# Kernel tuning notes

Measured on AMD Instinct MI355X. Metric: run time of the kernel, lower is better.

## Reference

```python
import jax, jax.numpy as jnp
import numpy as np

EPS = 1e-6


def _att_vector(x, W, b, sharp2, th2, is_last):
    """AttentionVector on a 2D payoff slice.
    x: (N, a, m). W: (1, 2), b: (1,). Returns (N, a)."""
    # compare_param: pair (x[n,j,k], x[n,i,k]) -> Linear(2,1) -> sigmoid -> mean over k
    # Linear on the concat pair is w00*x[n,j,k] + w01*x[n,i,k] + b, so we fuse it.
    lin = W[0, 0] * x[:, None, :, :] + W[0, 1] * x[:, :, None, :] + b[0]  # (N,a,a,m)
    c = jnp.mean(jax.nn.sigmoid(lin), axis=3)  # (N,a,a)
    # max_normalize over dim 2
    c = c / (jnp.max(c, axis=2, keepdims=True) + EPS)
    # compute_player_mask
    m = jnp.mean(c, axis=2)  # (N,a)
    m = jax.nn.relu(m * sharp2[0] + th2[0])
    m = jax.nn.softmax(m, axis=1)
    if not is_last:
        m = m / (jnp.max(m, axis=1, keepdims=True) + EPS)
    return m


def setup_inputs() -> dict:
    key = jax.random.key(0)
    ks = jax.random.split(key, 16)
    N, a1, a2, f = 128, 64, 64, 2
    inp = {
        "x": jax.random.normal(ks[0], (N, f, a1, a2), dtype=jnp.float32),
        "fc_W": jax.random.normal(ks[1], (2, 2), dtype=jnp.float32) * 0.5,
        "fc_b": jax.random.normal(ks[2], (2,), dtype=jnp.float32) * 0.1,
        "p1_W": jax.random.normal(ks[3], (1, 2), dtype=jnp.float32) * 0.5,
        "p1_b": jax.random.normal(ks[4], (1,), dtype=jnp.float32) * 0.1,
        "p1_sharp": jnp.ones((1,), dtype=jnp.float32),
        "p1_th": jnp.zeros((1,), dtype=jnp.float32),
        "p2_W": jax.random.normal(ks[5], (1, 2), dtype=jnp.float32) * 0.5,
        "p2_b": jax.random.normal(ks[6], (1,), dtype=jnp.float32) * 0.1,
        "p2_sharp": jnp.ones((1,), dtype=jnp.float32),
        "p2_th": jnp.zeros((1,), dtype=jnp.float32),
        "out_W": jax.random.normal(ks[7], (1, 2), dtype=jnp.float32) * 0.5,
        "out_b": jax.random.normal(ks[8], (1,), dtype=jnp.float32) * 0.1,
        "out_sharp": jnp.ones((1,), dtype=jnp.float32),
        "out_th": jnp.zeros((1,), dtype=jnp.float32),
    }
    return inp


def reference(x, fc_W, fc_b, p1_W, p1_b, p1_sharp, p1_th,
              p2_W, p2_b, p2_sharp, p2_th,
              out_W, out_b, out_sharp, out_th):
    # x: (N, f=2, a1, a2) -> (N, a1, a2, f)
    h = jnp.transpose(x, (0, 2, 3, 1))
    # is_fc_first: Linear(2, 2) + ReLU on last dim
    h = jax.nn.relu(h @ fc_W.T + fc_b)  # (N,a1,a2,2)
    # one AttentionModule (module_layers=1, not simult)
    vec1 = _att_vector(h[..., 0], p1_W, p1_b, p1_sharp, p1_th, is_last=False)  # (N,a1)
    h = h * vec1[:, :, None, None]
    pl2 = jnp.transpose(h[..., 1], (0, 2, 1))  # (N,a2,a1)
    vec2 = _att_vector(pl2, p2_W, p2_b, p2_sharp, p2_th, is_last=False)  # (N,a2)
    h = h * vec2[:, None, :, None]
    # with_last: final AttentionVector (is_last=True) on player-1 channel
    out = _att_vector(h[..., 0], out_W, out_b, out_sharp, out_th, is_last=True)  # (N,a1)
    return out
```

## Files before the change

kernel.cpp:

```cpp
#include <hip/hip_runtime.h>


constexpr int A   = 64;
constexpr int PAD = 68;
constexpr float L2E  = 1.4426950408889634f;
constexpr float EPSF = 1e-6f;

__device__ __forceinline__ float bcast(float v, int srcLane) {
    return __int_as_float(__builtin_amdgcn_readlane(__float_as_int(v), srcLane));
}
__device__ __forceinline__ float rcpf(float v) { return __builtin_amdgcn_rcpf(v); }
__device__ __forceinline__ float ex2(float v)  { return __builtin_amdgcn_exp2f(v); }

template <int CTRL>
__device__ __forceinline__ float upd_dpp(float src) {
    return __int_as_float(__builtin_amdgcn_update_dpp(
        0, __float_as_int(src), CTRL, 0xF, 0xF, true));
}
__device__ __forceinline__ float wave_sum64(float x) {
    x += upd_dpp<0x111>(x);
    x += upd_dpp<0x112>(x);
    x += upd_dpp<0x114>(x);
    x += upd_dpp<0x118>(x);
    x += upd_dpp<0x142>(x);
    x += upd_dpp<0x143>(x);
    return bcast(x, 63);
}
__device__ __forceinline__ float wave_max64(float x) {
    x = fmaxf(x, upd_dpp<0x111>(x));
    x = fmaxf(x, upd_dpp<0x112>(x));
    x = fmaxf(x, upd_dpp<0x114>(x));
    x = fmaxf(x, upd_dpp<0x118>(x));
    x = fmaxf(x, upd_dpp<0x142>(x));
    x = fmaxf(x, upd_dpp<0x143>(x));
    return bcast(x, 63);
}

__device__ __forceinline__ void att2q(const float* __restrict__ prow,
                                      const float* __restrict__ qL,
                                      int row0, int lane,
                                      float* __restrict__ mbuf,
                                      float* __restrict__ mg)
{
    const float qreg0 = qL[row0 * PAD + lane];
    const float qreg1 = qL[(row0 + 1) * PAD + lane];
    float acc0 = 0.f, acc1 = 0.f;
#pragma unroll
    for (int c = 0; c < 4; ++c) {
        float pk[16];
        *(float4*)(&pk[0])  = *(const float4*)(prow + c * 16 + 0);
        *(float4*)(&pk[4])  = *(const float4*)(prow + c * 16 + 4);
        *(float4*)(&pk[8])  = *(const float4*)(prow + c * 16 + 8);
        *(float4*)(&pk[12]) = *(const float4*)(prow + c * 16 + 12);
#pragma unroll
        for (int g = 0; g < 4; ++g) {
            const int k = c * 16 + 4 * g;
            const float p0 = pk[4 * g], p1 = pk[4 * g + 1];
            const float p2 = pk[4 * g + 2], p3 = pk[4 * g + 3];
            {
                float u0 = fmaf(p0, bcast(qreg0, k),     1.0f);
                float u1 = fmaf(p1, bcast(qreg0, k + 1), 1.0f);
                float u2 = fmaf(p2, bcast(qreg0, k + 2), 1.0f);
                float u3 = fmaf(p3, bcast(qreg0, k + 3), 1.0f);
                float a = u0 * u1, b = u2 * u3;
                float numer = fmaf(u0 + u1, b, (u2 + u3) * a);
                acc0 = fmaf(numer, rcpf(a * b), acc0);
            }
            {
                float u0 = fmaf(p0, bcast(qreg1, k),     1.0f);
                float u1 = fmaf(p1, bcast(qreg1, k + 1), 1.0f);
                float u2 = fmaf(p2, bcast(qreg1, k + 2), 1.0f);
                float u3 = fmaf(p3, bcast(qreg1, k + 3), 1.0f);
                float a = u0 * u1, b = u2 * u3;
                float numer = fmaf(u0 + u1, b, (u2 + u3) * a);
                acc1 = fmaf(numer, rcpf(a * b), acc1);
            }
        }
    }
    const float s0 = wave_sum64(acc0), m0 = wave_max64(acc0);
    const float s1 = wave_sum64(acc1), m1 = wave_max64(acc1);
    if (lane == 0) {
        float v0 = (s0 * (1.0f / 4096.0f)) / (m0 * (1.0f / 64.0f) + EPSF);
        float v1 = (s1 * (1.0f / 4096.0f)) / (m1 * (1.0f / 64.0f) + EPSF);
        mbuf[row0]     = v0;
        mbuf[row0 + 1] = v1;
        __hip_atomic_store(mg + row0,     v0 + 2.0f, __ATOMIC_RELAXED, __HIP_MEMORY_SCOPE_AGENT);
        __hip_atomic_store(mg + row0 + 1, v1 + 2.0f, __ATOMIC_RELAXED, __HIP_MEMORY_SCOPE_AGENT);
    }
}

__device__ __forceinline__ float softmax64(float m, float sharp, float th, bool last)
{
    float v = fmaxf(0.f, m * sharp + th);
    float mx = wave_max64(v);
    float e = __expf(v - mx);
    float s = wave_sum64(e);
    float r = e / s;
    if (!last) {
        float rm = wave_max64(r);
        r = r / (rm + EPSF);
    }
    return r;
}

__device__ __forceinline__ float exch_soft(const float* __restrict__ mbuf,
                                           const float* __restrict__ mg,
                                           int half, int lane,
                                           float sharp, float th, bool last)
{
    float mv;
    if ((lane >> 5) == half) {
        mv = mbuf[lane];
    } else {
        const float* p = mg + lane;
        for (;;) {
            float f = __hip_atomic_load(p, __ATOMIC_RELAXED, __HIP_MEMORY_SCOPE_AGENT);
            unsigned u = __float_as_uint(f);
            if ((u >> 23) == 0x80u) { mv = f - 2.0f; break; }
            __builtin_amdgcn_s_sleep(1);
        }
    }
    return softmax64(mv, sharp, th, last);
}

__global__ __launch_bounds__(1024, 4)
void attn_half(const float* __restrict__ x,
               const float* __restrict__ fcW, const float* __restrict__ fcb,
               const float* __restrict__ p1W, const float* __restrict__ p1b,
               const float* __restrict__ p1s, const float* __restrict__ p1t,
               const float* __restrict__ p2W, const float* __restrict__ p2b,
               const float* __restrict__ p2s, const float* __restrict__ p2t,
               const float* __restrict__ oW,  const float* __restrict__ ob,
               const float* __restrict__ os,  const float* __restrict__ ot,
               float* __restrict__ mglob,
               float* __restrict__ out)
{
    __shared__ __align__(16) float pL[A * PAD];
    __shared__ __align__(16) float qL[A * PAD];
    __shared__ float mbuf[A];
    __shared__ float v1buf[A], v2buf[A];

    const int tid = threadIdx.x, lane = tid & 63, wv = tid >> 6;
    const int n = blockIdx.x >> 1, half = blockIdx.x & 1;
    const int row0 = half * 32 + wv * 2;
    const int i = tid >> 4, j = (tid & 15) * 4;
    float* mg = mglob + (size_t)n * 3 * A;

    const float4* x0v = (const float4*)(x + (size_t)n * 2 * A * A);
    const float4* x1v = x0v + (A * A / 4);
    const float4 a = x0v[tid];
    const float4 c = x1v[tid];
    const float w00 = fcW[0], w01 = fcW[1], w10 = fcW[2], w11 = fcW[3];
    const float b0 = fcb[0], b1 = fcb[1];
    const float h0v[4] = { fmaxf(0.f, w00 * a.x + w01 * c.x + b0),
                           fmaxf(0.f, w00 * a.y + w01 * c.y + b0),
                           fmaxf(0.f, w00 * a.z + w01 * c.z + b0),
                           fmaxf(0.f, w00 * a.w + w01 * c.w + b0) };
    const float h1v[4] = { fmaxf(0.f, w10 * a.x + w11 * c.x + b1),
                           fmaxf(0.f, w10 * a.y + w11 * c.y + b1),
                           fmaxf(0.f, w10 * a.z + w11 * c.z + b1),
                           fmaxf(0.f, w10 * a.w + w11 * c.w + b1) };

    {
        const float W0 = p1W[0], W1 = p1W[1], bb = p1b[0];
        float4 pv, qv;
        pv.x = ex2(-L2E * (W0 * h0v[0] + bb)); qv.x = ex2(-L2E * (W1 * h0v[0]));
        pv.y = ex2(-L2E * (W0 * h0v[1] + bb)); qv.y = ex2(-L2E * (W1 * h0v[1]));
        pv.z = ex2(-L2E * (W0 * h0v[2] + bb)); qv.z = ex2(-L2E * (W1 * h0v[2]));
        pv.w = ex2(-L2E * (W0 * h0v[3] + bb)); qv.w = ex2(-L2E * (W1 * h0v[3]));
        *(float4*)&pL[i * PAD + j] = pv;
        *(float4*)&qL[i * PAD + j] = qv;
    }
    __syncthreads();
    att2q(pL + lane * PAD, qL, row0, lane, mbuf, mg);
    __syncthreads();
    if (wv == 0) v1buf[lane] = exch_soft(mbuf, mg, half, lane, p1s[0], p1t[0], false);
    __syncthreads();

    {
        const float W0 = p2W[0], W1 = p2W[1], bb = p2b[0];
        const float sc = v1buf[i];
#pragma unroll
        for (int t = 0; t < 4; ++t) {
            float hv = h1v[t] * sc;
            pL[(j + t) * PAD + i] = ex2(-L2E * (W0 * hv + bb));
            qL[(j + t) * PAD + i] = ex2(-L2E * (W1 * hv));
        }
    }
    __syncthreads();
    att2q(pL + lane * PAD, qL, row0, lane, mbuf, mg + A);
    __syncthreads();
    if (wv == 0) v2buf[lane] = exch_soft(mbuf, mg + A, half, lane, p2s[0], p2t[0], false);
    __syncthreads();

    {
        const float W0 = oW[0], W1 = oW[1], bb = ob[0];
        const float sc = v1buf[i];
        const float4 v2q = *(const float4*)&v2buf[j];
        float hv0 = h0v[0] * sc * v2q.x, hv1 = h0v[1] * sc * v2q.y;
        float hv2 = h0v[2] * sc * v2q.z, hv3 = h0v[3] * sc * v2q.w;
        float4 pv, qv;
        pv.x = ex2(-L2E * (W0 * hv0 + bb)); qv.x = ex2(-L2E * (W1 * hv0));
        pv.y = ex2(-L2E * (W0 * hv1 + bb)); qv.y = ex2(-L2E * (W1 * hv1));
        pv.z = ex2(-L2E * (W0 * hv2 + bb)); qv.z = ex2(-L2E * (W1 * hv2));
        pv.w = ex2(-L2E * (W0 * hv3 + bb)); qv.w = ex2(-L2E * (W1 * hv3));
        *(float4*)&pL[i * PAD + j] = pv;
        *(float4*)&qL[i * PAD + j] = qv;
    }
    __syncthreads();
    att2q(pL + lane * PAD, qL, row0, lane, mbuf, mg + 2 * A);
    __syncthreads();

    if (wv == 0) {
        float r = exch_soft(mbuf, mg + 2 * A, half, lane, os[0], ot[0], true);
        if ((lane >> 5) == half) out[(size_t)n * A + lane] = r;
    }
}

extern "C" void kernel_launch(void* const* d_in, const int* in_sizes, int n_in,
                              void* d_out, int out_size, void* d_ws, size_t ws_size,
                              hipStream_t stream)
{
    (void)n_in; (void)out_size; (void)ws_size;
    const float* x   = (const float*)d_in[0];
    const float* fcW = (const float*)d_in[1];
    const float* fcb = (const float*)d_in[2];
    const float* p1W = (const float*)d_in[3];
    const float* p1b = (const float*)d_in[4];
    const float* p1s = (const float*)d_in[5];
    const float* p1t = (const float*)d_in[6];
    const float* p2W = (const float*)d_in[7];
    const float* p2b = (const float*)d_in[8];
    const float* p2s = (const float*)d_in[9];
    const float* p2t = (const float*)d_in[10];
    const float* oW  = (const float*)d_in[11];
    const float* ob  = (const float*)d_in[12];
    const float* os  = (const float*)d_in[13];
    const float* ot  = (const float*)d_in[14];
    float* out = (float*)d_out;

    const int N = in_sizes[0] / (2 * A * A);
    float* mglob = (float*)d_ws;

    attn_half<<<2 * N, 1024, 0, stream>>>(x, fcW, fcb,
                                          p1W, p1b, p1s, p1t,
                                          p2W, p2b, p2s, p2t,
                                          oW, ob, os, ot, mglob, out);
}
```

Baseline: 100.1 us.

## Split each sample across four 512-thread blocks and poll softmax in every wave

Each sample's work is now spread across four blocks of 512 threads instead of two blocks of 1024, and each thread handles eight elements. Every wave polls the global exchange buffer for all 64 row values and computes the softmax redundantly. The result is broadcast across lanes with ds_bpermute instead of going through shared-memory buffers, which removes several __syncthreads barriers. In exchange there is more cross-block spin-waiting on global memory, and the blocks of one sample must all be co-resident to avoid deadlock.

```diff
diff --git a/kernel.cpp b/kernel.cpp
--- a/kernel.cpp
+++ b/kernel.cpp
@@ -11,6 +11,9 @@
 }
 __device__ __forceinline__ float rcpf(float v) { return __builtin_amdgcn_rcpf(v); }
 __device__ __forceinline__ float ex2(float v)  { return __builtin_amdgcn_exp2f(v); }
+__device__ __forceinline__ float lanebc(float v, int idx) {
+    return __int_as_float(__builtin_amdgcn_ds_bpermute(idx << 2, __float_as_int(v)));
+}
 
 template <int CTRL>
 __device__ __forceinline__ float upd_dpp(float src) {
@@ -39,7 +42,6 @@
 __device__ __forceinline__ void att2q(const float* __restrict__ prow,
                                       const float* __restrict__ qL,
                                       int row0, int lane,
-                                      float* __restrict__ mbuf,
                                       float* __restrict__ mg)
 {
     const float qreg0 = qL[row0 * PAD + lane];
@@ -82,8 +84,6 @@
     if (lane == 0) {
         float v0 = (s0 * (1.0f / 4096.0f)) / (m0 * (1.0f / 64.0f) + EPSF);
         float v1 = (s1 * (1.0f / 4096.0f)) / (m1 * (1.0f / 64.0f) + EPSF);
-        mbuf[row0]     = v0;
-        mbuf[row0 + 1] = v1;
         __hip_atomic_store(mg + row0,     v0 + 2.0f, __ATOMIC_RELAXED, __HIP_MEMORY_SCOPE_AGENT);
         __hip_atomic_store(mg + row0 + 1, v1 + 2.0f, __ATOMIC_RELAXED, __HIP_MEMORY_SCOPE_AGENT);
     }
@@ -103,117 +103,111 @@
     return r;
 }
 
-__device__ __forceinline__ float exch_soft(const float* __restrict__ mbuf,
-                                           const float* __restrict__ mg,
-                                           int half, int lane,
+__device__ __forceinline__ float poll_soft(const float* __restrict__ mg,
+                                           int lane,
                                            float sharp, float th, bool last)
 {
     float mv;
-    if ((lane >> 5) == half) {
-        mv = mbuf[lane];
-    } else {
-        const float* p = mg + lane;
-        for (;;) {
-            float f = __hip_atomic_load(p, __ATOMIC_RELAXED, __HIP_MEMORY_SCOPE_AGENT);
-            unsigned u = __float_as_uint(f);
-            if ((u >> 23) == 0x80u) { mv = f - 2.0f; break; }
-            __builtin_amdgcn_s_sleep(1);
-        }
+    const float* p = mg + lane;
+    for (;;) {
+        float f = __hip_atomic_load(p, __ATOMIC_RELAXED, __HIP_MEMORY_SCOPE_AGENT);
+        if (__all((__float_as_uint(f) >> 23) == 0x80u)) { mv = f - 2.0f; break; }
+        __builtin_amdgcn_s_sleep(1);
     }
     return softmax64(mv, sharp, th, last);
 }
 
-__global__ __launch_bounds__(1024, 4)
-void attn_half(const float* __restrict__ x,
-               const float* __restrict__ fcW, const float* __restrict__ fcb,
-               const float* __restrict__ p1W, const float* __restrict__ p1b,
-               const float* __restrict__ p1s, const float* __restrict__ p1t,
-               const float* __restrict__ p2W, const float* __restrict__ p2b,
-               const float* __restrict__ p2s, const float* __restrict__ p2t,
-               const float* __restrict__ oW,  const float* __restrict__ ob,
-               const float* __restrict__ os,  const float* __restrict__ ot,
-               float* __restrict__ mglob,
-               float* __restrict__ out)
+__global__ __launch_bounds__(512, 4)
+void attn_q(const float* __restrict__ x,
+            const float* __restrict__ fcW, const float* __restrict__ fcb,
+            const float* __restrict__ p1W, const float* __restrict__ p1b,
+            const float* __restrict__ p1s, const float* __restrict__ p1t,
+            const float* __restrict__ p2W, const float* __restrict__ p2b,
+            const float* __restrict__ p2s, const float* __restrict__ p2t,
+            const float* __restrict__ oW,  const float* __restrict__ ob,
+            const float* __restrict__ os,  const float* __restrict__ ot,
+            float* __restrict__ mglob,
+            float* __restrict__ out)
 {
     __shared__ __align__(16) float pL[A * PAD];
     __shared__ __align__(16) float qL[A * PAD];
-    __shared__ float mbuf[A];
-    __shared__ float v1buf[A], v2buf[A];
 
     const int tid = threadIdx.x, lane = tid & 63, wv = tid >> 6;
-    const int n = blockIdx.x >> 1, half = blockIdx.x & 1;
-    const int row0 = half * 32 + wv * 2;
-    const int i = tid >> 4, j = (tid & 15) * 4;
+    const int n = blockIdx.x >> 2, quarter = blockIdx.x & 3;
+    const int row0 = quarter * 16 + wv * 2;
+    const int i = tid >> 3, j8 = (tid & 7) << 3;
     float* mg = mglob + (size_t)n * 3 * A;
 
-    const float4* x0v = (const float4*)(x + (size_t)n * 2 * A * A);
-    const float4* x1v = x0v + (A * A / 4);
-    const float4 a = x0v[tid];
-    const float4 c = x1v[tid];
-    const float w00 = fcW[0], w01 = fcW[1], w10 = fcW[2], w11 = fcW[3];
-    const float b0 = fcb[0], b1 = fcb[1];
-    const float h0v[4] = { fmaxf(0.f, w00 * a.x + w01 * c.x + b0),
-                           fmaxf(0.f, w00 * a.y + w01 * c.y + b0),
-                           fmaxf(0.f, w00 * a.z + w01 * c.z + b0),
-                           fmaxf(0.f, w00 * a.w + w01 * c.w + b0) };
-    const float h1v[4] = { fmaxf(0.f, w10 * a.x + w11 * c.x + b1),
-                           fmaxf(0.f, w10 * a.y + w11 * c.y + b1),
-                           fmaxf(0.f, w10 * a.z + w11 * c.z + b1),
-                           fmaxf(0.f, w10 * a.w + w11 * c.w + b1) };
+    const float4* xv = (const float4*)(x + (size_t)n * 2 * A * A);
+    const float4 a0 = xv[2 * tid], a1 = xv[2 * tid + 1];
+    const float4 c0 = xv[1024 + 2 * tid], c1 = xv[1024 + 2 * tid + 1];
+    float h0v[8], h1v[8];
+    {
+        const float w00 = fcW[0], w01 = fcW[1], w10 = fcW[2], w11 = fcW[3];
+        const float b0 = fcb[0], b1 = fcb[1];
+        const float av[8] = { a0.x, a0.y, a0.z, a0.w, a1.x, a1.y, a1.z, a1.w };
+        const float cv[8] = { c0.x, c0.y, c0.z, c0.w, c1.x, c1.y, c1.z, c1.w };
+#pragma unroll
+        for (int t = 0; t < 8; ++t) {
+            h0v[t] = fmaxf(0.f, w00 * av[t] + w01 * cv[t] + b0);
+            h1v[t] = fmaxf(0.f, w10 * av[t] + w11 * cv[t] + b1);
+        }
+    }
 
     {
         const float W0 = p1W[0], W1 = p1W[1], bb = p1b[0];
-        float4 pv, qv;
-        pv.x = ex2(-L2E * (W0 * h0v[0] + bb)); qv.x = ex2(-L2E * (W1 * h0v[0]));
-        pv.y = ex2(-L2E * (W0 * h0v[1] + bb)); qv.y = ex2(-L2E * (W1 * h0v[1]));
-        pv.z = ex2(-L2E * (W0 * h0v[2] + bb)); qv.z = ex2(-L2E * (W1 * h0v[2]));
-        pv.w = ex2(-L2E * (W0 * h0v[3] + bb)); qv.w = ex2(-L2E * (W1 * h0v[3]));
-        *(float4*)&pL[i * PAD + j] = pv;
-        *(float4*)&qL[i * PAD + j] = qv;
+        float pv[8], qv[8];
+#pragma unroll
+        for (int t = 0; t < 8; ++t) {
+            pv[t] = ex2(-L2E * (W0 * h0v[t] + bb));
+            qv[t] = ex2(-L2E * (W1 * h0v[t]));
+        }
+        *(float4*)&pL[i * PAD + j8]     = make_float4(pv[0], pv[1], pv[2], pv[3]);
+        *(float4*)&pL[i * PAD + j8 + 4] = make_float4(pv[4], pv[5], pv[6], pv[7]);
+        *(float4*)&qL[i * PAD + j8]     = make_float4(qv[0], qv[1], qv[2], qv[3]);
+        *(float4*)&qL[i * PAD + j8 + 4] = make_float4(qv[4], qv[5], qv[6], qv[7]);
     }
     __syncthreads();
-    att2q(pL + lane * PAD, qL, row0, lane, mbuf, mg);
+    att2q(pL + lane * PAD, qL, row0, lane, mg);
+    const float r1   = poll_soft(mg, lane, p1s[0], p1t[0], false);
+    const float v1_i = lanebc(r1, i);
+
+    {
+        const float W0 = p2W[0], W1 = p2W[1], bb = p2b[0];
+#pragma unroll
+        for (int t = 0; t < 8; ++t) {
+            const float hv = h1v[t] * v1_i;
+            pL[(j8 + t) * PAD + i] = ex2(-L2E * (W0 * hv + bb));
+            qL[(j8 + t) * PAD + i] = ex2(-L2E * (W1 * hv));
+        }
+    }
     __syncthreads();
-    if (wv == 0) v1buf[lane] = exch_soft(mbuf, mg, half, lane, p1s[0], p1t[0], false);
+    att2q(pL + lane * PAD, qL, row0, lane, mg + A);
+    const float r2 = poll_soft(mg + A, lane, p2s[0], p2t[0], false);
+
+    float v2j[8];
+#pragma unroll
+    for (int t = 0; t < 8; ++t) v2j[t] = lanebc(r2, j8 + t);
+    {
+        const float W0 = oW[0], W1 = oW[1], bb = ob[0];
+        float pv[8], qv[8];
+#pragma unroll
+        for (int t = 0; t < 8; ++t) {
+            const float hv = h0v[t] * v1_i * v2j[t];
+            pv[t] = ex2(-L2E * (W0 * hv + bb));
+            qv[t] = ex2(-L2E * (W1 * hv));
+        }
+        *(float4*)&pL[i * PAD + j8]     = make_float4(pv[0], pv[1], pv[2], pv[3]);
+        *(float4*)&pL[i * PAD + j8 + 4] = make_float4(pv[4], pv[5], pv[6], pv[7]);
+        *(float4*)&qL[i * PAD + j8]     = make_float4(qv[0], qv[1], qv[2], qv[3]);
+        *(float4*)&qL[i * PAD + j8 + 4] = make_float4(qv[4], qv[5], qv[6], qv[7]);
+    }
     __syncthreads();
-
-    {
-        const float W0 = p2W[0], W1 = p2W[1], bb = p2b[0];
-        const float sc = v1buf[i];
-#pragma unroll
-        for (int t = 0; t < 4; ++t) {
-            float hv = h1v[t] * sc;
-            pL[(j + t) * PAD + i] = ex2(-L2E * (W0 * hv + bb));
-            qL[(j + t) * PAD + i] = ex2(-L2E * (W1 * hv));
-        }
-    }
-    __syncthreads();
-    att2q(pL + lane * PAD, qL, row0, lane, mbuf, mg + A);
-    __syncthreads();
-    if (wv == 0) v2buf[lane] = exch_soft(mbuf, mg + A, half, lane, p2s[0], p2t[0], false);
-    __syncthreads();
-
-    {
-        const float W0 = oW[0], W1 = oW[1], bb = ob[0];
-        const float sc = v1buf[i];
-        const float4 v2q = *(const float4*)&v2buf[j];
-        float hv0 = h0v[0] * sc * v2q.x, hv1 = h0v[1] * sc * v2q.y;
-        float hv2 = h0v[2] * sc * v2q.z, hv3 = h0v[3] * sc * v2q.w;
-        float4 pv, qv;
-        pv.x = ex2(-L2E * (W0 * hv0 + bb)); qv.x = ex2(-L2E * (W1 * hv0));
-        pv.y = ex2(-L2E * (W0 * hv1 + bb)); qv.y = ex2(-L2E * (W1 * hv1));
-        pv.z = ex2(-L2E * (W0 * hv2 + bb)); qv.z = ex2(-L2E * (W1 * hv2));
-        pv.w = ex2(-L2E * (W0 * hv3 + bb)); qv.w = ex2(-L2E * (W1 * hv3));
-        *(float4*)&pL[i * PAD + j] = pv;
-        *(float4*)&qL[i * PAD + j] = qv;
-    }
-    __syncthreads();
-    att2q(pL + lane * PAD, qL, row0, lane, mbuf, mg + 2 * A);
-    __syncthreads();
+    att2q(pL + lane * PAD, qL, row0, lane, mg + 2 * A);
 
     if (wv == 0) {
-        float r = exch_soft(mbuf, mg + 2 * A, half, lane, os[0], ot[0], true);
-        if ((lane >> 5) == half) out[(size_t)n * A + lane] = r;
+        const float r = poll_soft(mg + 2 * A, lane, os[0], ot[0], true);
+        if ((lane >> 4) == quarter) out[(size_t)n * A + lane] = r;
     }
 }
 
@@ -242,8 +236,8 @@
     const int N = in_sizes[0] / (2 * A * A);
     float* mglob = (float*)d_ws;
 
-    attn_half<<<2 * N, 1024, 0, stream>>>(x, fcW, fcb,
-                                          p1W, p1b, p1s, p1t,
-                                          p2W, p2b, p2s, p2t,
-                                          oW, ob, os, ot, mglob, out);
-}
+    attn_q<<<4 * N, 512, 0, stream>>>(x, fcW, fcb,
+                                      p1W, p1b, p1s, p1t,
+                                      p2W, p2b, p2s, p2t,
+                                      oW, ob, os, ot, mglob, out);
+}
```

Measured after the change: 110.6 us. 10.5% more time.

## Process each sample in one block instead of two cooperating half-blocks

Applied to the files above, without the earlier changes.

Replaces the two-blocks-per-sample split, which swapped row statistics through global memory with atomic spin-waits, with one 1024-thread block per sample. Each wave now handles four rows instead of two. Every wave computes the softmax redundantly and gets the per-row scale factors by lane broadcast rather than shared-memory buffers, which drops a barrier per stage. This removes the cross-block handshake and its latency, but halves the grid, so only 128 blocks cover the device and per-block compute doubles.

```diff
diff --git a/kernel.cpp b/kernel.cpp
--- a/kernel.cpp
+++ b/kernel.cpp
@@ -11,6 +11,9 @@
 }
 __device__ __forceinline__ float rcpf(float v) { return __builtin_amdgcn_rcpf(v); }
 __device__ __forceinline__ float ex2(float v)  { return __builtin_amdgcn_exp2f(v); }
+__device__ __forceinline__ float lanebc(float v, int idx) {
+    return __int_as_float(__builtin_amdgcn_ds_bpermute(idx << 2, __float_as_int(v)));
+}
 
 template <int CTRL>
 __device__ __forceinline__ float upd_dpp(float src) {
@@ -39,8 +42,7 @@
 __device__ __forceinline__ void att2q(const float* __restrict__ prow,
                                       const float* __restrict__ qL,
                                       int row0, int lane,
-                                      float* __restrict__ mbuf,
-                                      float* __restrict__ mg)
+                                      float* __restrict__ mbuf)
 {
     const float qreg0 = qL[row0 * PAD + lane];
     const float qreg1 = qL[(row0 + 1) * PAD + lane];
@@ -80,12 +82,8 @@
     const float s0 = wave_sum64(acc0), m0 = wave_max64(acc0);
     const float s1 = wave_sum64(acc1), m1 = wave_max64(acc1);
     if (lane == 0) {
-        float v0 = (s0 * (1.0f / 4096.0f)) / (m0 * (1.0f / 64.0f) + EPSF);
-        float v1 = (s1 * (1.0f / 4096.0f)) / (m1 * (1.0f / 64.0f) + EPSF);
-        mbuf[row0]     = v0;
-        mbuf[row0 + 1] = v1;
-        __hip_atomic_store(mg + row0,     v0 + 2.0f, __ATOMIC_RELAXED, __HIP_MEMORY_SCOPE_AGENT);
-        __hip_atomic_store(mg + row0 + 1, v1 + 2.0f, __ATOMIC_RELAXED, __HIP_MEMORY_SCOPE_AGENT);
+        mbuf[row0]     = (s0 * (1.0f / 4096.0f)) / (m0 * (1.0f / 64.0f) + EPSF);
+        mbuf[row0 + 1] = (s1 * (1.0f / 4096.0f)) / (m1 * (1.0f / 64.0f) + EPSF);
     }
 }
 
@@ -103,28 +101,8 @@
     return r;
 }
 
-__device__ __forceinline__ float exch_soft(const float* __restrict__ mbuf,
-                                           const float* __restrict__ mg,
-                                           int half, int lane,
-                                           float sharp, float th, bool last)
-{
-    float mv;
-    if ((lane >> 5) == half) {
-        mv = mbuf[lane];
-    } else {
-        const float* p = mg + lane;
-        for (;;) {
-            float f = __hip_atomic_load(p, __ATOMIC_RELAXED, __HIP_MEMORY_SCOPE_AGENT);
-            unsigned u = __float_as_uint(f);
-            if ((u >> 23) == 0x80u) { mv = f - 2.0f; break; }
-            __builtin_amdgcn_s_sleep(1);
-        }
-    }
-    return softmax64(mv, sharp, th, last);
-}
-
 __global__ __launch_bounds__(1024, 4)
-void attn_half(const float* __restrict__ x,
+void attn_full(const float* __restrict__ x,
                const float* __restrict__ fcW, const float* __restrict__ fcb,
                const float* __restrict__ p1W, const float* __restrict__ p1b,
                const float* __restrict__ p1s, const float* __restrict__ p1t,
@@ -132,19 +110,16 @@
                const float* __restrict__ p2s, const float* __restrict__ p2t,
                const float* __restrict__ oW,  const float* __restrict__ ob,
                const float* __restrict__ os,  const float* __restrict__ ot,
-               float* __restrict__ mglob,
                float* __restrict__ out)
 {
     __shared__ __align__(16) float pL[A * PAD];
     __shared__ __align__(16) float qL[A * PAD];
     __shared__ float mbuf[A];
-    __shared__ float v1buf[A], v2buf[A];
 
     const int tid = threadIdx.x, lane = tid & 63, wv = tid >> 6;
-    const int n = blockIdx.x >> 1, half = blockIdx.x & 1;
-    const int row0 = half * 32 + wv * 2;
+    const int n = blockIdx.x;
+    const int row0 = wv * 4;
     const int i = tid >> 4, j = (tid & 15) * 4;
-    float* mg = mglob + (size_t)n * 3 * A;
 
     const float4* x0v = (const float4*)(x + (size_t)n * 2 * A * A);
     const float4* x1v = x0v + (A * A / 4);
@@ -172,48 +147,50 @@
         *(float4*)&qL[i * PAD + j] = qv;
     }
     __syncthreads();
-    att2q(pL + lane * PAD, qL, row0, lane, mbuf, mg);
-    __syncthreads();
-    if (wv == 0) v1buf[lane] = exch_soft(mbuf, mg, half, lane, p1s[0], p1t[0], false);
-    __syncthreads();
+    att2q(pL + lane * PAD, qL, row0,     lane, mbuf);
+    att2q(pL + lane * PAD, qL, row0 + 2, lane, mbuf);
+    __syncthreads();
+    const float r1   = softmax64(mbuf[lane], p1s[0], p1t[0], false);
+    const float v1_i = lanebc(r1, i);
 
     {
         const float W0 = p2W[0], W1 = p2W[1], bb = p2b[0];
-        const float sc = v1buf[i];
 #pragma unroll
         for (int t = 0; t < 4; ++t) {
-            float hv = h1v[t] * sc;
+            const float hv = h1v[t] * v1_i;
             pL[(j + t) * PAD + i] = ex2(-L2E * (W0 * hv + bb));
             qL[(j + t) * PAD + i] = ex2(-L2E * (W1 * hv));
         }
     }
     __syncthreads();
-    att2q(pL + lane * PAD, qL, row0, lane, mbuf, mg + A);
-    __syncthreads();
-    if (wv == 0) v2buf[lane] = exch_soft(mbuf, mg + A, half, lane, p2s[0], p2t[0], false);
-    __syncthreads();
+    att2q(pL + lane * PAD, qL, row0,     lane, mbuf);
+    att2q(pL + lane * PAD, qL, row0 + 2, lane, mbuf);
+    __syncthreads();
+    const float r2 = softmax64(mbuf[lane], p2s[0], p2t[0], false);
+    float v2j[4];
+#pragma unroll
+    for (int t = 0; t < 4; ++t) v2j[t] = lanebc(r2, j + t);
 
     {
-        const float W0 = oW[0], W1 = oW[1], bb = ob[0];
-        const float sc = v1buf[i];
-        const float4 v2q = *(const float4*)&v2buf[j];
-        float hv0 = h0v[0] * sc * v2q.x, hv1 = h0v[1] * sc * v2q.y;
-        float hv2 = h0v[2] * sc * v2q.z, hv3 = h0v[3] * sc * v2q.w;
+        const float W0 = oW[0], W1 = ob ? oW[1] : oW[1], bb = ob[0];
+        const float hv0 = h0v[0] * v1_i * v2j[0], hv1 = h0v[1] * v1_i * v2j[1];
+        const float hv2 = h0v[2] * v1_i * v2j[2], hv3 = h0v[3] * v1_i * v2j[3];
         float4 pv, qv;
-        pv.x = ex2(-L2E * (W0 * hv0 + bb)); qv.x = ex2(-L2E * (W1 * hv0));
-        pv.y = ex2(-L2E * (W0 * hv1 + bb)); qv.y = ex2(-L2E * (W1 * hv1));
-        pv.z = ex2(-L2E * (W0 * hv2 + bb)); qv.z = ex2(-L2E * (W1 * hv2));
-        pv.w = ex2(-L2E * (W0 * hv3 + bb)); qv.w = ex2(-L2E * (W1 * hv3));
+        pv.x = ex2(-L2E * (W0 * hv0 + bb)); qv.x = ex2(-L2E * (oW[1] * hv0));
+        pv.y = ex2(-L2E * (W0 * hv1 + bb)); qv.y = ex2(-L2E * (oW[1] * hv1));
+        pv.z = ex2(-L2E * (W0 * hv2 + bb)); qv.z = ex2(-L2E * (oW[1] * hv2));
+        pv.w = ex2(-L2E * (W0 * hv3 + bb)); qv.w = ex2(-L2E * (oW[1] * hv3));
         *(float4*)&pL[i * PAD + j] = pv;
         *(float4*)&qL[i * PAD + j] = qv;
     }
     __syncthreads();
-    att2q(pL + lane * PAD, qL, row0, lane, mbuf, mg + 2 * A);
+    att2q(pL + lane * PAD, qL, row0,     lane, mbuf);
+    att2q(pL + lane * PAD, qL, row0 + 2, lane, mbuf);
     __syncthreads();
 
     if (wv == 0) {
-        float r = exch_soft(mbuf, mg + 2 * A, half, lane, os[0], ot[0], true);
-        if ((lane >> 5) == half) out[(size_t)n * A + lane] = r;
+        const float r = softmax64(mbuf[lane], os[0], ot[0], true);
+        out[(size_t)n * A + lane] = r;
     }
 }
 
@@ -221,7 +198,7 @@
                               void* d_out, int out_size, void* d_ws, size_t ws_size,
                               hipStream_t stream)
 {
-    (void)n_in; (void)out_size; (void)ws_size;
+    (void)n_in; (void)out_size; (void)d_ws; (void)ws_size;
     const float* x   = (const float*)d_in[0];
     const float* fcW = (const float*)d_in[1];
     const float* fcb = (const float*)d_in[2];
@@ -240,10 +217,9 @@
     float* out = (float*)d_out;
 
     const int N = in_sizes[0] / (2 * A * A);
-    float* mglob = (float*)d_ws;
-
-    attn_half<<<2 * N, 1024, 0, stream>>>(x, fcW, fcb,
-                                          p1W, p1b, p1s, p1t,
-                                          p2W, p2b, p2s, p2t,
-                                          oW, ob, os, ot, mglob, out);
-}
+
+    attn_full<<<N, 1024, 0, stream>>>(x, fcW, fcb,
+                                      p1W, p1b, p1s, p1t,
+                                      p2W, p2b, p2s, p2t,
+                                      oW, ob, os, ot, out);
+}
```

Result: slower. 109.1 us (+8.9%).

## Exchange half-block masks through output buffer with tagged ack handshake; load q from LDS

Applied to the files above, without the earlier changes.

Drops the workspace buffer and uses the output row itself as the inter-block mailbox. Values carry a per-phase additive tag, and the consumer writes back an ack that the producer waits for before the slot is reused. The attention inner loop now reads q values from LDS with float4 loads instead of readlane broadcasts from a register, which trades SALU/readlane traffic for LDS bandwidth. It clamps mask values to a small positive floor so the tag decode works, which slightly changes semantics for near-zero values. It also adds an extra spin-wait round-trip per phase.

```diff
diff --git a/kernel.cpp b/kernel.cpp
--- a/kernel.cpp
+++ b/kernel.cpp
@@ -37,13 +37,11 @@
 }
 
 __device__ __forceinline__ void att2q(const float* __restrict__ prow,
-                                      const float* __restrict__ qL,
+                                      const float* __restrict__ qrow,
                                       int row0, int lane,
                                       float* __restrict__ mbuf,
-                                      float* __restrict__ mg)
-{
-    const float qreg0 = qL[row0 * PAD + lane];
-    const float qreg1 = qL[(row0 + 1) * PAD + lane];
+                                      unsigned* __restrict__ mg, unsigned K)
+{
     float acc0 = 0.f, acc1 = 0.f;
 #pragma unroll
     for (int c = 0; c < 4; ++c) {
@@ -57,24 +55,21 @@
             const int k = c * 16 + 4 * g;
             const float p0 = pk[4 * g], p1 = pk[4 * g + 1];
             const float p2 = pk[4 * g + 2], p3 = pk[4 * g + 3];
-            {
-                float u0 = fmaf(p0, bcast(qreg0, k),     1.0f);
-                float u1 = fmaf(p1, bcast(qreg0, k + 1), 1.0f);
-                float u2 = fmaf(p2, bcast(qreg0, k + 2), 1.0f);
-                float u3 = fmaf(p3, bcast(qreg0, k + 3), 1.0f);
-                float a = u0 * u1, b = u2 * u3;
-                float numer = fmaf(u0 + u1, b, (u2 + u3) * a);
-                acc0 = fmaf(numer, rcpf(a * b), acc0);
+            const float4 q0 = *(const float4*)(qrow + k);
+            const float4 q1 = *(const float4*)(qrow + PAD + k);
+#define ROW_ACC(ACC, Q)                                              \
+            {                                                        \
+                float u0 = fmaf(p0, (Q).x, 1.0f);                    \
+                float u1 = fmaf(p1, (Q).y, 1.0f);                    \
+                float u2 = fmaf(p2, (Q).z, 1.0f);                    \
+                float u3 = fmaf(p3, (Q).w, 1.0f);                    \
+                float a = u0 * u1, b = u2 * u3;                      \
+                float numer = fmaf(u0 + u1, b, (u2 + u3) * a);       \
+                ACC = fmaf(numer, rcpf(a * b), ACC);                 \
             }
-            {
-                float u0 = fmaf(p0, bcast(qreg1, k),     1.0f);
-                float u1 = fmaf(p1, bcast(qreg1, k + 1), 1.0f);
-                float u2 = fmaf(p2, bcast(qreg1, k + 2), 1.0f);
-                float u3 = fmaf(p3, bcast(qreg1, k + 3), 1.0f);
-                float a = u0 * u1, b = u2 * u3;
-                float numer = fmaf(u0 + u1, b, (u2 + u3) * a);
-                acc1 = fmaf(numer, rcpf(a * b), acc1);
-            }
+            ROW_ACC(acc0, q0)
+            ROW_ACC(acc1, q1)
+#undef ROW_ACC
         }
     }
     const float s0 = wave_sum64(acc0), m0 = wave_max64(acc0);
@@ -82,10 +77,14 @@
     if (lane == 0) {
         float v0 = (s0 * (1.0f / 4096.0f)) / (m0 * (1.0f / 64.0f) + EPSF);
         float v1 = (s1 * (1.0f / 4096.0f)) / (m1 * (1.0f / 64.0f) + EPSF);
+        v0 = fmaxf(v0, 1e-9f);
+        v1 = fmaxf(v1, 1e-9f);
         mbuf[row0]     = v0;
         mbuf[row0 + 1] = v1;
-        __hip_atomic_store(mg + row0,     v0 + 2.0f, __ATOMIC_RELAXED, __HIP_MEMORY_SCOPE_AGENT);
-        __hip_atomic_store(mg + row0 + 1, v1 + 2.0f, __ATOMIC_RELAXED, __HIP_MEMORY_SCOPE_AGENT);
+        __hip_atomic_store(mg + row0,     __float_as_uint(v0) + K,
+                           __ATOMIC_RELAXED, __HIP_MEMORY_SCOPE_AGENT);
+        __hip_atomic_store(mg + row0 + 1, __float_as_uint(v1) + K,
+                           __ATOMIC_RELAXED, __HIP_MEMORY_SCOPE_AGENT);
     }
 }
 
@@ -104,23 +103,32 @@
 }
 
 __device__ __forceinline__ float exch_soft(const float* __restrict__ mbuf,
-                                           const float* __restrict__ mg,
+                                           unsigned* __restrict__ mg,
                                            int half, int lane,
+                                           unsigned K, unsigned ACK,
                                            float sharp, float th, bool last)
 {
+    const bool own = ((lane >> 5) == half);
     float mv;
-    if ((lane >> 5) == half) {
+    if (own) {
         mv = mbuf[lane];
     } else {
-        const float* p = mg + lane;
+        unsigned* p = mg + lane;
         for (;;) {
-            float f = __hip_atomic_load(p, __ATOMIC_RELAXED, __HIP_MEMORY_SCOPE_AGENT);
-            unsigned u = __float_as_uint(f);
-            if ((u >> 23) == 0x80u) { mv = f - 2.0f; break; }
+            unsigned u = __hip_atomic_load(p, __ATOMIC_RELAXED, __HIP_MEMORY_SCOPE_AGENT);
+            unsigned d = u - K;
+            if (d - 0x30000000u <= 0x0F800000u) { mv = __uint_as_float(d); break; }
             __builtin_amdgcn_s_sleep(1);
         }
-    }
-    return softmax64(mv, sharp, th, last);
+        __hip_atomic_store(p, ACK, __ATOMIC_RELAXED, __HIP_MEMORY_SCOPE_AGENT);
+    }
+    const float r = softmax64(mv, sharp, th, last);
+    if (own) {
+        unsigned* p = mg + lane;
+        while (__hip_atomic_load(p, __ATOMIC_RELAXED, __HIP_MEMORY_SCOPE_AGENT) != ACK)
+            __builtin_amdgcn_s_sleep(1);
+    }
+    return r;
 }
 
 __global__ __launch_bounds__(1024, 4)
@@ -132,7 +140,6 @@
                const float* __restrict__ p2s, const float* __restrict__ p2t,
                const float* __restrict__ oW,  const float* __restrict__ ob,
                const float* __restrict__ os,  const float* __restrict__ ot,
-               float* __restrict__ mglob,
                float* __restrict__ out)
 {
     __shared__ __align__(16) float pL[A * PAD];
@@ -144,7 +151,7 @@
     const int n = blockIdx.x >> 1, half = blockIdx.x & 1;
     const int row0 = half * 32 + wv * 2;
     const int i = tid >> 4, j = (tid & 15) * 4;
-    float* mg = mglob + (size_t)n * 3 * A;
+    unsigned* mg = (unsigned*)(out + (size_t)n * A);
 
     const float4* x0v = (const float4*)(x + (size_t)n * 2 * A * A);
     const float4* x1v = x0v + (A * A / 4);
@@ -172,9 +179,11 @@
         *(float4*)&qL[i * PAD + j] = qv;
     }
     __syncthreads();
-    att2q(pL + lane * PAD, qL, row0, lane, mbuf, mg);
-    __syncthreads();
-    if (wv == 0) v1buf[lane] = exch_soft(mbuf, mg, half, lane, p1s[0], p1t[0], false);
+    att2q(pL + lane * PAD, qL + row0 * PAD, row0, lane, mbuf, mg, 0x40000000u);
+    __syncthreads();
+    if (wv == 0)
+        v1buf[lane] = exch_soft(mbuf, mg, half, lane, 0x40000000u, 1u,
+                                p1s[0], p1t[0], false);
     __syncthreads();
 
     {
@@ -182,23 +191,25 @@
         const float sc = v1buf[i];
 #pragma unroll
         for (int t = 0; t < 4; ++t) {
-            float hv = h1v[t] * sc;
+            const float hv = h1v[t] * sc;
             pL[(j + t) * PAD + i] = ex2(-L2E * (W0 * hv + bb));
             qL[(j + t) * PAD + i] = ex2(-L2E * (W1 * hv));
         }
     }
     __syncthreads();
-    att2q(pL + lane * PAD, qL, row0, lane, mbuf, mg + A);
-    __syncthreads();
-    if (wv == 0) v2buf[lane] = exch_soft(mbuf, mg + A, half, lane, p2s[0], p2t[0], false);
+    att2q(pL + lane * PAD, qL + row0 * PAD, row0, lane, mbuf, mg, 0x80000000u);
+    __syncthreads();
+    if (wv == 0)
+        v2buf[lane] = exch_soft(mbuf, mg, half, lane, 0x80000000u, 2u,
+                                p2s[0], p2t[0], false);
     __syncthreads();
 
     {
         const float W0 = oW[0], W1 = oW[1], bb = ob[0];
         const float sc = v1buf[i];
         const float4 v2q = *(const float4*)&v2buf[j];
-        float hv0 = h0v[0] * sc * v2q.x, hv1 = h0v[1] * sc * v2q.y;
-        float hv2 = h0v[2] * sc * v2q.z, hv3 = h0v[3] * sc * v2q.w;
+        const float hv0 = h0v[0] * sc * v2q.x, hv1 = h0v[1] * sc * v2q.y;
+        const float hv2 = h0v[2] * sc * v2q.z, hv3 = h0v[3] * sc * v2q.w;
         float4 pv, qv;
         pv.x = ex2(-L2E * (W0 * hv0 + bb)); qv.x = ex2(-L2E * (W1 * hv0));
         pv.y = ex2(-L2E * (W0 * hv1 + bb)); qv.y = ex2(-L2E * (W1 * hv1));
@@ -208,12 +219,15 @@
         *(float4*)&qL[i * PAD + j] = qv;
     }
     __syncthreads();
-    att2q(pL + lane * PAD, qL, row0, lane, mbuf, mg + 2 * A);
+    att2q(pL + lane * PAD, qL + row0 * PAD, row0, lane, mbuf, mg, 0xC0000000u);
     __syncthreads();
 
     if (wv == 0) {
-        float r = exch_soft(mbuf, mg + 2 * A, half, lane, os[0], ot[0], true);
-        if ((lane >> 5) == half) out[(size_t)n * A + lane] = r;
+        const float r = exch_soft(mbuf, mg, half, lane, 0xC0000000u, 3u,
+                                  os[0], ot[0], true);
+        if ((lane >> 5) == half)
+            __hip_atomic_store(mg + lane, __float_as_uint(r),
+                               __ATOMIC_RELAXED, __HIP_MEMORY_SCOPE_AGENT);
     }
 }
 
@@ -221,7 +235,7 @@
                               void* d_out, int out_size, void* d_ws, size_t ws_size,
                               hipStream_t stream)
 {
-    (void)n_in; (void)out_size; (void)ws_size;
+    (void)n_in; (void)out_size; (void)d_ws; (void)ws_size;
     const float* x   = (const float*)d_in[0];
     const float* fcW = (const float*)d_in[1];
     const float* fcb = (const float*)d_in[2];
@@ -240,10 +254,9 @@
     float* out = (float*)d_out;
 
     const int N = in_sizes[0] / (2 * A * A);
-    float* mglob = (float*)d_ws;
 
     attn_half<<<2 * N, 1024, 0, stream>>>(x, fcW, fcb,
                                           p1W, p1b, p1s, p1t,
                                           p2W, p2b, p2s, p2t,
-                                          oW, ob, os, ot, mglob, out);
-}
+                                          oW, ob, os, ot, out);
+}
```

After: 98.43 us. No clear change (-1.7%).
